# Performance work log

Measured on AMD Instinct MI355X. Metric: run time of the kernel, lower is better.

Reference implementation:

```python
import jax, jax.numpy as jnp
import numpy as np
from jax import lax

B, H, T, K = 32, 384, 1024, 3
MAX_LEN = 4096  # fixed ragged-output capacity (pad/mask for jit)
EPS = 1e-5


def conv1d_same(x, W, b):
    # x: [B,H,T], W: [H_out,H_in,K] -> [B,H,T] with SAME padding
    y = lax.conv_general_dilated(x, W, (1,), 'SAME',
                                 dimension_numbers=('NCH', 'OIH', 'NCH'))
    return y + b[None, :, None]


def layernorm_ch(x, g, b):
    # LayerNorm over the channel (hidden) dim of [B,H,T]
    m = jnp.mean(x, axis=1, keepdims=True)
    v = jnp.var(x, axis=1, keepdims=True)
    return (x - m) * lax.rsqrt(v + EPS) * g[None, :, None] + b[None, :, None]


def setup_inputs() -> dict:
    key = jax.random.key(0)
    ks = jax.random.split(key, 4)
    s = 0.02  # small init so floor(exp(relu(z))) gives modest durations
    x = jax.random.normal(ks[0], (B, H, T), dtype=jnp.float32)
    W1 = jax.random.normal(ks[1], (H, H, K), dtype=jnp.float32) * s
    W2 = jax.random.normal(ks[2], (H, H, K), dtype=jnp.float32) * s
    Wl = jax.random.normal(ks[3], (H, 1), dtype=jnp.float32) * s
    z = jnp.zeros((H,), jnp.float32)
    o = jnp.ones((H,), jnp.float32)
    return {'x': x, 'W1': W1, 'b1': z, 'g1': o, 'be1': z,
            'W2': W2, 'b2': z, 'g2': o, 'be2': z,
            'Wl': Wl, 'bl': jnp.zeros((1,), jnp.float32)}


def reference(x, W1, b1, g1, be1, W2, b2, g2, be2, Wl, bl):
    h = jax.nn.relu(layernorm_ch(conv1d_same(x, W1, b1), g1, be1))
    h = jax.nn.relu(layernorm_ch(conv1d_same(h, W2, b2), g2, be2))
    # Linear(H,1) applied per timestep, then ReLU
    z = jax.nn.relu(jnp.einsum('bht,h->bt', h, Wl[:, 0]) + bl[0])  # [B,T]
    durations = jnp.floor(jnp.exp(z)).astype(jnp.int32)            # [B,T]
    # ragged repeat_interleave along time, padded to MAX_LEN:
    cum = jnp.cumsum(durations, axis=-1)                           # [B,T]
    pos = jnp.arange(MAX_LEN)
    idx = jax.vmap(lambda c: jnp.searchsorted(c, pos, side='right'))(cum)  # [B,MAX]
    valid = (pos[None, :] < cum[:, -1:]).astype(x.dtype)           # [B,MAX]
    idx_c = jnp.minimum(idx, T - 1)
    aligned = jnp.take_along_axis(x, idx_c[:, None, :], axis=-1) * valid[:, None, :]
    return durations, aligned
```

## Files before the change

kernel.cpp:

```cpp
#include <hip/hip_runtime.h>
#include <hip/hip_bf16.h>


#define BB 32
#define HHD 384
#define TTOT 1024
#define MAXL 4096

typedef _Float16 half8 __attribute__((ext_vector_type(8)));
typedef float floatx4 __attribute__((ext_vector_type(4)));

__global__ void prep_w_kernel(const float* __restrict__ W1,
                              const float* __restrict__ W2,
                              _Float16* __restrict__ q1h, _Float16* __restrict__ q1l,
                              _Float16* __restrict__ q2h, _Float16* __restrict__ q2l) {
    const int e = blockIdx.x * 256 + threadIdx.x;
    const float* W = blockIdx.y ? W2 : W1;
    _Float16* oh = blockIdx.y ? q2h : q1h;
    _Float16* ol = blockIdx.y ? q2l : q1l;
    const int d  = e & 31;
    const int m  = (e >> 5) % 384;
    const int ck = e / (32 * 384);
    const int c  = ck / 3, k = ck - 3 * c;
    const float w = W[(size_t)m * 1152 + (size_t)(32 * c + d) * 3 + k];
    const _Float16 hi = (_Float16)w;
    oh[e] = hi;
    ol[e] = (_Float16)((w - (float)hi) * 2048.0f);
}

__global__ void prep_x_kernel(const float* __restrict__ X,
                              _Float16* __restrict__ o1,
                              _Float16* __restrict__ o2) {
    __shared__ float Ls[64][65];
    const int h0 = blockIdx.x * 64;
    const int t0 = blockIdx.y * 64;
    const int b  = blockIdx.z;
    const int tid = threadIdx.x;
    const int tl = tid & 63, hq = tid >> 6;
    const float* Xb = X + (size_t)b * HHD * TTOT;
#pragma unroll
    for (int i = 0; i < 16; ++i) {
        const int h = i * 4 + hq;
        Ls[tl][h] = Xb[(size_t)(h0 + h) * TTOT + t0 + tl];
    }
    __syncthreads();
#pragma unroll
    for (int i = 0; i < 16; ++i) {
        const int t = i * 4 + hq;
        const float v = Ls[t][tl];
        const _Float16 a = (_Float16)v;
        const size_t o = ((size_t)b * TTOT + t0 + t) * HHD + h0 + tl;
        o1[o] = a;
        o2[o] = (_Float16)((v - (float)a) * 2048.0f);
    }
}

__launch_bounds__(256, 2)
__global__ void conv_mfma_kernel(const _Float16* __restrict__ Bh,
                                 const _Float16* __restrict__ Bl,
                                 const _Float16* __restrict__ Ah,
                                 const _Float16* __restrict__ Al,
                                 const float* __restrict__ bias,
                                 float* __restrict__ Out) {
    __shared__ __align__(16) _Float16 sm[33440];
    const int tid  = threadIdx.x;
    const int lane = tid & 63, wid = tid >> 6;
    const int wm = wid >> 1, wn = wid & 1;
    const int l15 = lane & 15, g4 = lane >> 4;
    const int h0 = blockIdx.x * 96;
    const int t0 = blockIdx.y * 128;
    const int b  = blockIdx.z;

    floatx4 ahh[3][4], axx[3][4];
#pragma unroll
    for (int mt = 0; mt < 3; ++mt)
#pragma unroll
        for (int nt = 0; nt < 4; ++nt) {
            ahh[mt][nt] = (floatx4){0.f, 0.f, 0.f, 0.f};
            axx[mt][nt] = (floatx4){0.f, 0.f, 0.f, 0.f};
        }

    const size_t xbase = (size_t)b * TTOT * HHD;

    for (int ch = 0; ch < 12; ++ch) {
        __syncthreads();
#pragma unroll
        for (int it = 0; it < 9; ++it) {
            const int e  = tid + it * 256;
            const int s  = e / 1152;
            const int r1 = e - s * 1152;
            const int k  = r1 / 384;
            const int q  = r1 - k * 384;
            const int m  = q >> 2, c8 = (q & 3) << 3;
            const _Float16* src = (s ? Al : Ah) +
                ((size_t)((ch * 3 + k) * 384 + h0 + m) << 5) + c8;
            const uint4 v = *(const uint4*)src;
            *(uint4*)&sm[((s * 3 + k) * 96 + m) * 40 + c8] = v;
        }
#pragma unroll
        for (int it = 0; it < 5; ++it) {
            const int e = tid + it * 256;
            if (e < 1040) {
                const int s  = e / 520;
                const int r1 = e - s * 520;
                const int j  = r1 >> 2, q = r1 & 3;
                const int gt = t0 - 1 + j;
                uint4 v = make_uint4(0u, 0u, 0u, 0u);
                if (gt >= 0 && gt < TTOT) {
                    const _Float16* src = (s ? Bl : Bh) + xbase +
                        (size_t)gt * HHD + ch * 32 + (q << 3);
                    v = *(const uint4*)src;
                }
                *(uint4*)&sm[23040 + (s * 130 + j) * 40 + (q << 3)] = v;
            }
        }
        __syncthreads();

#pragma unroll
        for (int k = 0; k < 3; ++k) {
            half8 ah[3], al[3], bh[4], bl[4];
#pragma unroll
            for (int mt = 0; mt < 3; ++mt) {
                const int m = wm * 48 + mt * 16 + l15;
                ah[mt] = *(const half8*)&sm[((0 + k) * 96 + m) * 40 + g4 * 8];
                al[mt] = *(const half8*)&sm[((3 + k) * 96 + m) * 40 + g4 * 8];
            }
#pragma unroll
            for (int nt = 0; nt < 4; ++nt) {
                const int j = wn * 64 + nt * 16 + l15 + k;
                bh[nt] = *(const half8*)&sm[23040 + (0   + j) * 40 + g4 * 8];
                bl[nt] = *(const half8*)&sm[23040 + (130 + j) * 40 + g4 * 8];
            }
#pragma unroll
            for (int mt = 0; mt < 3; ++mt)
#pragma unroll
                for (int nt = 0; nt < 4; ++nt) {
                    ahh[mt][nt] = __builtin_amdgcn_mfma_f32_16x16x32_f16(
                        ah[mt], bh[nt], ahh[mt][nt], 0, 0, 0);
                    axx[mt][nt] = __builtin_amdgcn_mfma_f32_16x16x32_f16(
                        ah[mt], bl[nt], axx[mt][nt], 0, 0, 0);
                    axx[mt][nt] = __builtin_amdgcn_mfma_f32_16x16x32_f16(
                        al[mt], bh[nt], axx[mt][nt], 0, 0, 0);
                }
        }
    }

    __syncthreads();
    float* Lt = (float*)sm;
#pragma unroll
    for (int mt = 0; mt < 3; ++mt)
#pragma unroll
        for (int nt = 0; nt < 4; ++nt) {
            const int row = wn * 64 + nt * 16 + l15;
            const int col = wm * 48 + mt * 16 + g4 * 4;
            float4 v;
            v.x = ahh[mt][nt][0] + axx[mt][nt][0] * (1.0f / 2048.0f);
            v.y = ahh[mt][nt][1] + axx[mt][nt][1] * (1.0f / 2048.0f);
            v.z = ahh[mt][nt][2] + axx[mt][nt][2] * (1.0f / 2048.0f);
            v.w = ahh[mt][nt][3] + axx[mt][nt][3] * (1.0f / 2048.0f);
            *(float4*)&Lt[row * 100 + col] = v;
        }
    __syncthreads();
    const size_t obase = ((size_t)b * TTOT + t0) * HHD + h0;
#pragma unroll
    for (int i = 0; i < 12; ++i) {
        const int e = tid + i * 256;
        const int row = e / 24, c4 = (e - row * 24) * 4;
        float4 v = *(const float4*)&Lt[row * 100 + c4];
        const float4 bv = *(const float4*)&bias[h0 + c4];
        v.x += bv.x; v.y += bv.y; v.z += bv.z; v.w += bv.w;
        *(float4*)&Out[obase + (size_t)row * HHD + c4] = v;
    }
}

__global__ void ln_split_kernel(const float* __restrict__ hraw,
                                const float* __restrict__ g,
                                const float* __restrict__ be,
                                _Float16* __restrict__ o1,
                                _Float16* __restrict__ o2) {
    const int row = blockIdx.x * 4 + (threadIdx.x >> 6);
    const int ln  = threadIdx.x & 63;
    const float* src = hraw + (size_t)row * HHD;
    float v[6], s = 0.f, ss = 0.f;
#pragma unroll
    for (int j = 0; j < 6; ++j) { v[j] = src[ln + 64 * j]; s += v[j]; ss += v[j] * v[j]; }
#pragma unroll
    for (int m = 32; m >= 1; m >>= 1) { s += __shfl_xor(s, m, 64); ss += __shfl_xor(ss, m, 64); }
    const float mean = s * (1.f / HHD);
    const float var  = ss * (1.f / HHD) - mean * mean;
    const float inv  = rsqrtf(var + 1e-5f);
#pragma unroll
    for (int j = 0; j < 6; ++j) {
        const int h = ln + 64 * j;
        float y = (v[j] - mean) * inv * g[h] + be[h];
        y = fmaxf(y, 0.f);
        const _Float16 a = (_Float16)y;
        const size_t o = (size_t)row * HHD + h;
        o1[o] = a;
        o2[o] = (_Float16)((y - (float)a) * 2048.0f);
    }
}

__global__ void ln_proj_kernel(const float* __restrict__ hraw,
                               const float* __restrict__ g,
                               const float* __restrict__ be,
                               const float* __restrict__ Wl,
                               const float* __restrict__ blp,
                               float* __restrict__ zb) {
    const int row = blockIdx.x * 4 + (threadIdx.x >> 6);
    const int ln  = threadIdx.x & 63;
    const float* src = hraw + (size_t)row * HHD;
    float v[6], s = 0.f, ss = 0.f;
#pragma unroll
    for (int j = 0; j < 6; ++j) { v[j] = src[ln + 64 * j]; s += v[j]; ss += v[j] * v[j]; }
#pragma unroll
    for (int m = 32; m >= 1; m >>= 1) { s += __shfl_xor(s, m, 64); ss += __shfl_xor(ss, m, 64); }
    const float mean = s * (1.f / HHD);
    const float inv  = rsqrtf(ss * (1.f / HHD) - mean * mean + 1e-5f);
    float zs = 0.f;
#pragma unroll
    for (int j = 0; j < 6; ++j) {
        const int h = ln + 64 * j;
        float y = (v[j] - mean) * inv * g[h] + be[h];
        zs += fmaxf(y, 0.f) * Wl[h];
    }
#pragma unroll
    for (int m = 32; m >= 1; m >>= 1) zs += __shfl_xor(zs, m, 64);
    if (ln == 0) zb[row] = fmaxf(zs + blp[0], 0.f);
}

__global__ void dur_scan_kernel(const float* __restrict__ z,
                                float* __restrict__ durOut,
                                int* __restrict__ cum) {
    __shared__ int sb[TTOT];
    const int b = blockIdx.x;
    const int t = threadIdx.x;
    const int d = (int)floorf(expf(z[b * TTOT + t]));
    durOut[b * TTOT + t] = (float)d;
    sb[t] = d;
    __syncthreads();
    for (int off = 1; off < TTOT; off <<= 1) {
        const int v = (t >= off) ? sb[t - off] : 0;
        __syncthreads();
        sb[t] += v;
        __syncthreads();
    }
    cum[b * TTOT + t] = sb[t];
}

__global__ void gather_kernel(const float* __restrict__ X,
                              const int* __restrict__ cum,
                              float* __restrict__ aligned) {
    __shared__ int cs[TTOT];
    const int b   = blockIdx.y;
    const int tid = threadIdx.x;
    for (int e = tid; e < TTOT; e += 256) cs[e] = cum[b * TTOT + e];
    __syncthreads();
    const int pos   = blockIdx.x * 256 + tid;
    const int total = cs[TTOT - 1];
    int lo = 0, hi = TTOT;
    while (lo < hi) {
        const int mid = (lo + hi) >> 1;
        if (cs[mid] <= pos) lo = mid + 1; else hi = mid;
    }
    const float vmul = (pos < total) ? 1.f : 0.f;
    const int idx = min(lo, TTOT - 1);
    const float* Xb = X + (size_t)b * HHD * TTOT;
    float* Ab = aligned + (size_t)b * HHD * MAXL;
#pragma unroll 4
    for (int h = 0; h < HHD; ++h)
        Ab[(size_t)h * MAXL + pos] = Xb[(size_t)h * TTOT + idx] * vmul;
}

extern "C" void kernel_launch(void* const* d_in, const int* in_sizes, int n_in,
                              void* d_out, int out_size, void* d_ws, size_t ws_size,
                              hipStream_t stream) {
    const float* x   = (const float*)d_in[0];
    const float* W1  = (const float*)d_in[1];
    const float* b1  = (const float*)d_in[2];
    const float* g1  = (const float*)d_in[3];
    const float* be1 = (const float*)d_in[4];
    const float* W2  = (const float*)d_in[5];
    const float* b2  = (const float*)d_in[6];
    const float* g2  = (const float*)d_in[7];
    const float* be2 = (const float*)d_in[8];
    const float* Wl  = (const float*)d_in[9];
    const float* bl  = (const float*)d_in[10];

    float* out     = (float*)d_out;
    float* durOut  = out;
    float* aligned = out + (size_t)BB * TTOT;
    float* h_raw   = aligned;

    char* ws = (char*)d_ws;
    const size_t wqB = (size_t)442368 * sizeof(_Float16);
    const size_t xtB = (size_t)BB * TTOT * HHD * sizeof(_Float16);
    _Float16* Wq1h = (_Float16*)(ws);
    _Float16* Wq1l = (_Float16*)(ws + wqB);
    _Float16* Wq2h = (_Float16*)(ws + 2 * wqB);
    _Float16* Wq2l = (_Float16*)(ws + 3 * wqB);
    _Float16* Xt1  = (_Float16*)(ws + 4 * wqB);
    _Float16* Xt2  = (_Float16*)(ws + 4 * wqB + xtB);
    float*    zb   = (float*)   (ws + 4 * wqB + 2 * xtB);
    int*      cum  = (int*)     (ws + 4 * wqB + 2 * xtB + (size_t)BB * TTOT * 4);

    prep_w_kernel<<<dim3(1728, 2), 256, 0, stream>>>(W1, W2, Wq1h, Wq1l, Wq2h, Wq2l);
    prep_x_kernel<<<dim3(6, 16, 32), 256, 0, stream>>>(x, Xt1, Xt2);
    conv_mfma_kernel<<<dim3(4, 8, 32), 256, 0, stream>>>(Xt1, Xt2, Wq1h, Wq1l, b1, h_raw);
    ln_split_kernel<<<8192, 256, 0, stream>>>(h_raw, g1, be1, Xt1, Xt2);
    conv_mfma_kernel<<<dim3(4, 8, 32), 256, 0, stream>>>(Xt1, Xt2, Wq2h, Wq2l, b2, h_raw);
    ln_proj_kernel<<<8192, 256, 0, stream>>>(h_raw, g2, be2, Wl, bl, zb);
    dur_scan_kernel<<<BB, TTOT, 0, stream>>>(zb, durOut, cum);
    gather_kernel<<<dim3(MAXL / 256, BB), 256, 0, stream>>>(x, cum, aligned);
}
```

Baseline: 515.8 us.

## Prefetch next chunk's weight and input tiles into registers during MFMA compute

The conv GEMM kernel's global-to-LDS staging becomes register-staged software pipelining. The next channel chunk's weight and input tiles are loaded into registers while the current chunk's MFMAs run, and the address arithmetic is hoisted out of the loop. This hides global load latency behind compute at the cost of about 56 extra VGPRs per thread, which may lower occupancy.

```diff
diff --git a/kernel.cpp b/kernel.cpp
--- a/kernel.cpp
+++ b/kernel.cpp
@@ -82,39 +82,68 @@
 
     const size_t xbase = (size_t)b * TTOT * HHD;
 
+    int wdst[9];
+    const _Float16* wsrc0[9];
+#pragma unroll
+    for (int it = 0; it < 9; ++it) {
+        const int e  = tid + it * 256;
+        const int s  = e / 1152;
+        const int r1 = e - s * 1152;
+        const int k  = r1 / 384;
+        const int q  = r1 - k * 384;
+        const int m  = q >> 2, c8 = (q & 3) << 3;
+        wsrc0[it] = (s ? Al : Ah) + ((size_t)(k * 384 + h0 + m) << 5) + c8;
+        wdst[it]  = ((s * 3 + k) * 96 + m) * 40 + c8;
+    }
+    int xdst[5], xgt[5];
+    const _Float16* xsrc0[5];
+    bool xact[5];
+#pragma unroll
+    for (int it = 0; it < 5; ++it) {
+        const int e = tid + it * 256;
+        xact[it] = (e < 1040);
+        const int s  = e / 520;
+        const int r1 = e - s * 520;
+        const int j  = r1 >> 2, q = r1 & 3;
+        const int gt = t0 - 1 + j;
+        xgt[it]  = gt;
+        xsrc0[it] = (s ? Bl : Bh) + xbase + (size_t)max(gt, 0) * HHD + (q << 3);
+        xdst[it]  = 23040 + (s * 130 + j) * 40 + (q << 3);
+    }
+
+    uint4 wreg[9], xreg[5];
+#pragma unroll
+    for (int it = 0; it < 9; ++it) wreg[it] = *(const uint4*)(wsrc0[it]);
+#pragma unroll
+    for (int it = 0; it < 5; ++it) {
+        uint4 v = make_uint4(0u, 0u, 0u, 0u);
+        if (xact[it] && xgt[it] >= 0 && xgt[it] < TTOT)
+            v = *(const uint4*)(xsrc0[it]);
+        xreg[it] = v;
+    }
+
     for (int ch = 0; ch < 12; ++ch) {
         __syncthreads();
 #pragma unroll
-        for (int it = 0; it < 9; ++it) {
-            const int e  = tid + it * 256;
-            const int s  = e / 1152;
-            const int r1 = e - s * 1152;
-            const int k  = r1 / 384;
-            const int q  = r1 - k * 384;
-            const int m  = q >> 2, c8 = (q & 3) << 3;
-            const _Float16* src = (s ? Al : Ah) +
-                ((size_t)((ch * 3 + k) * 384 + h0 + m) << 5) + c8;
-            const uint4 v = *(const uint4*)src;
-            *(uint4*)&sm[((s * 3 + k) * 96 + m) * 40 + c8] = v;
-        }
-#pragma unroll
-        for (int it = 0; it < 5; ++it) {
-            const int e = tid + it * 256;
-            if (e < 1040) {
-                const int s  = e / 520;
-                const int r1 = e - s * 520;
-                const int j  = r1 >> 2, q = r1 & 3;
-                const int gt = t0 - 1 + j;
+        for (int it = 0; it < 9; ++it) *(uint4*)&sm[wdst[it]] = wreg[it];
+#pragma unroll
+        for (int it = 0; it < 5; ++it)
+            if (xact[it]) *(uint4*)&sm[xdst[it]] = xreg[it];
+        __syncthreads();
+
+        if (ch < 11) {
+            const size_t woff = (size_t)(ch + 1) * 3 * 384 * 32;
+            const int    xoff = (ch + 1) * 32;
+#pragma unroll
+            for (int it = 0; it < 9; ++it) wreg[it] = *(const uint4*)(wsrc0[it] + woff);
+#pragma unroll
+            for (int it = 0; it < 5; ++it) {
                 uint4 v = make_uint4(0u, 0u, 0u, 0u);
-                if (gt >= 0 && gt < TTOT) {
-                    const _Float16* src = (s ? Bl : Bh) + xbase +
-                        (size_t)gt * HHD + ch * 32 + (q << 3);
-                    v = *(const uint4*)src;
-                }
-                *(uint4*)&sm[23040 + (s * 130 + j) * 40 + (q << 3)] = v;
+                if (xact[it] && xgt[it] >= 0 && xgt[it] < TTOT)
+                    v = *(const uint4*)(xsrc0[it] + xoff);
+                xreg[it] = v;
             }
         }
-        __syncthreads();
 
 #pragma unroll
         for (int k = 0; k < 3; ++k) {
```

Measured after the change: 639.8 us. 24.1% more time.

## Use direct global-to-LDS loads for conv tiles and mask halo in registers

Applied to the files above, without the earlier changes.

Replaces the register-staged global→LDS copies of weight and input tiles with global_load_lds direct transfers, precomputing source pointers outside the channel loop. The LDS layout drops the 40-element padded row stride for an unpadded 32 stride, because direct loads write contiguous per-wave chunks. Out-of-range time halo rows are now loaded from clamped addresses and zeroed in registers at the MFMA operand stage. This cuts VGPR traffic and LDS footprint, but the unpadded stride may cause LDS bank conflicts on the half8 reads.

```diff
diff --git a/kernel.cpp b/kernel.cpp
--- a/kernel.cpp
+++ b/kernel.cpp
@@ -62,7 +62,7 @@
                                  const _Float16* __restrict__ Al,
                                  const float* __restrict__ bias,
                                  float* __restrict__ Out) {
-    __shared__ __align__(16) _Float16 sm[33440];
+    __shared__ __align__(16) _Float16 sm[26752];
     const int tid  = threadIdx.x;
     const int lane = tid & 63, wid = tid >> 6;
     const int wm = wid >> 1, wn = wid & 1;
@@ -70,6 +70,10 @@
     const int h0 = blockIdx.x * 96;
     const int t0 = blockIdx.y * 128;
     const int b  = blockIdx.z;
+    const int wbid = tid & 192;
+
+    const bool haloL = (blockIdx.y == 0) && (wn == 0) && (l15 == 0);
+    const bool haloH = (blockIdx.y == 7) && (wn == 1) && (l15 == 15);
 
     floatx4 ahh[3][4], axx[3][4];
 #pragma unroll
@@ -82,37 +86,51 @@
 
     const size_t xbase = (size_t)b * TTOT * HHD;
 
+    const _Float16* wsrc[9];
+#pragma unroll
+    for (int it = 0; it < 9; ++it) {
+        const int e  = tid + it * 256;
+        const int s  = e / 1152;
+        const int r1 = e - s * 1152;
+        const int k  = r1 / 384;
+        const int q  = r1 - k * 384;
+        const int m  = q >> 2, c8 = (q & 3) << 3;
+        wsrc[it] = (s ? Al : Ah) + ((size_t)(k * 384 + h0 + m) << 5) + c8;
+    }
+    const _Float16* xsrc[5];
+#pragma unroll
+    for (int it = 0; it < 5; ++it) {
+        const int e  = tid + it * 256;
+        const int s  = e / 520;
+        const int r1 = e - s * 520;
+        const int j  = r1 >> 2, q = r1 & 3;
+        const int gt  = t0 - 1 + j;
+        const int gtc = min(max(gt, 0), TTOT - 1);
+        xsrc[it] = (s ? Bl : Bh) + xbase + (size_t)gtc * HHD + (q << 3);
+    }
+
+    const half8 hz = {0, 0, 0, 0, 0, 0, 0, 0};
+
     for (int ch = 0; ch < 12; ++ch) {
         __syncthreads();
+        const size_t woff = (size_t)ch * (3 * 384 * 32);
+        const int    xoff = ch * 32;
 #pragma unroll
         for (int it = 0; it < 9; ++it) {
-            const int e  = tid + it * 256;
-            const int s  = e / 1152;
-            const int r1 = e - s * 1152;
-            const int k  = r1 / 384;
-            const int q  = r1 - k * 384;
-            const int m  = q >> 2, c8 = (q & 3) << 3;
-            const _Float16* src = (s ? Al : Ah) +
-                ((size_t)((ch * 3 + k) * 384 + h0 + m) << 5) + c8;
-            const uint4 v = *(const uint4*)src;
-            *(uint4*)&sm[((s * 3 + k) * 96 + m) * 40 + c8] = v;
-        }
-#pragma unroll
-        for (int it = 0; it < 5; ++it) {
-            const int e = tid + it * 256;
-            if (e < 1040) {
-                const int s  = e / 520;
-                const int r1 = e - s * 520;
-                const int j  = r1 >> 2, q = r1 & 3;
-                const int gt = t0 - 1 + j;
-                uint4 v = make_uint4(0u, 0u, 0u, 0u);
-                if (gt >= 0 && gt < TTOT) {
-                    const _Float16* src = (s ? Bl : Bh) + xbase +
-                        (size_t)gt * HHD + ch * 32 + (q << 3);
-                    v = *(const uint4*)src;
-                }
-                *(uint4*)&sm[23040 + (s * 130 + j) * 40 + (q << 3)] = v;
-            }
+            __builtin_amdgcn_global_load_lds(
+                (const unsigned int*)(wsrc[it] + woff),
+                (unsigned int*)&sm[(size_t)(it * 256 + wbid) * 8], 16, 0, 0);
+        }
+#pragma unroll
+        for (int it = 0; it < 4; ++it) {
+            __builtin_amdgcn_global_load_lds(
+                (const unsigned int*)(xsrc[it] + xoff),
+                (unsigned int*)&sm[18432 + (size_t)(it * 256 + wbid) * 8], 16, 0, 0);
+        }
+        if (tid < 16) {
+            __builtin_amdgcn_global_load_lds(
+                (const unsigned int*)(xsrc[4] + xoff),
+                (unsigned int*)&sm[18432 + (size_t)(4 * 256) * 8], 16, 0, 0);
         }
         __syncthreads();
 
@@ -122,15 +140,17 @@
 #pragma unroll
             for (int mt = 0; mt < 3; ++mt) {
                 const int m = wm * 48 + mt * 16 + l15;
-                ah[mt] = *(const half8*)&sm[((0 + k) * 96 + m) * 40 + g4 * 8];
-                al[mt] = *(const half8*)&sm[((3 + k) * 96 + m) * 40 + g4 * 8];
+                ah[mt] = *(const half8*)&sm[((0 + k) * 96 + m) * 32 + g4 * 8];
+                al[mt] = *(const half8*)&sm[((3 + k) * 96 + m) * 32 + g4 * 8];
             }
 #pragma unroll
             for (int nt = 0; nt < 4; ++nt) {
                 const int j = wn * 64 + nt * 16 + l15 + k;
-                bh[nt] = *(const half8*)&sm[23040 + (0   + j) * 40 + g4 * 8];
-                bl[nt] = *(const half8*)&sm[23040 + (130 + j) * 40 + g4 * 8];
+                bh[nt] = *(const half8*)&sm[18432 + (0   + j) * 32 + g4 * 8];
+                bl[nt] = *(const half8*)&sm[18432 + (130 + j) * 32 + g4 * 8];
             }
+            if (k == 0 && haloL) { bh[0] = hz; bl[0] = hz; }
+            if (k == 2 && haloH) { bh[3] = hz; bl[3] = hz; }
 #pragma unroll
             for (int mt = 0; mt < 3; ++mt)
 #pragma unroll
```

After: 484.2 us. 1.07x faster.

## Fuse conv with channel LayerNorm by giving each block all channels

Applied to the files above, without the earlier changes.

The conv kernel now computes all 384 output channels for a 32-timestep tile, so LayerNorm statistics can be reduced inside the block. The first LayerNorm, ReLU and hi/lo fp16 split are folded into the first conv's epilogue, and the second LayerNorm plus the linear projection into the second's. This removes the fp32 intermediate round-trips through global memory and two separate LN launches. Weight and activation tiles are now staged with direct global-to-LDS loads, and the weight tile is reloaded per tap with extra barriers. The trade-offs are a smaller time tile with more weight traffic per block and only 1024 blocks.

```diff
diff --git a/kernel.cpp b/kernel.cpp
--- a/kernel.cpp
+++ b/kernel.cpp
@@ -55,86 +55,103 @@
     }
 }
 
+template <int MODE>
 __launch_bounds__(256, 2)
-__global__ void conv_mfma_kernel(const _Float16* __restrict__ Bh,
-                                 const _Float16* __restrict__ Bl,
-                                 const _Float16* __restrict__ Ah,
-                                 const _Float16* __restrict__ Al,
-                                 const float* __restrict__ bias,
-                                 float* __restrict__ Out) {
-    __shared__ __align__(16) _Float16 sm[33440];
+__global__ void conv_ln_fused(const _Float16* __restrict__ Bh,
+                              const _Float16* __restrict__ Bl,
+                              const _Float16* __restrict__ Ah,
+                              const _Float16* __restrict__ Al,
+                              const float* __restrict__ bias,
+                              const float* __restrict__ gain,
+                              const float* __restrict__ beta,
+                              const float* __restrict__ Wl,
+                              const float* __restrict__ blp,
+                              _Float16* __restrict__ O1,
+                              _Float16* __restrict__ O2,
+                              float* __restrict__ zb) {
+    __shared__ __align__(16) _Float16 sm[26752];
     const int tid  = threadIdx.x;
-    const int lane = tid & 63, wid = tid >> 6;
-    const int wm = wid >> 1, wn = wid & 1;
+    const int lane = tid & 63, w = tid >> 6;
     const int l15 = lane & 15, g4 = lane >> 4;
-    const int h0 = blockIdx.x * 96;
-    const int t0 = blockIdx.y * 128;
-    const int b  = blockIdx.z;
-
-    floatx4 ahh[3][4], axx[3][4];
-#pragma unroll
-    for (int mt = 0; mt < 3; ++mt)
-#pragma unroll
-        for (int nt = 0; nt < 4; ++nt) {
+    const int tt = blockIdx.x;
+    const int t0 = tt * 32;
+    const int b  = blockIdx.y;
+
+    floatx4 ahh[6][2], axx[6][2];
+#pragma unroll
+    for (int mt = 0; mt < 6; ++mt)
+#pragma unroll
+        for (int nt = 0; nt < 2; ++nt) {
             ahh[mt][nt] = (floatx4){0.f, 0.f, 0.f, 0.f};
             axx[mt][nt] = (floatx4){0.f, 0.f, 0.f, 0.f};
         }
 
     const size_t xbase = (size_t)b * TTOT * HHD;
-
-    for (int ch = 0; ch < 12; ++ch) {
-        __syncthreads();
-#pragma unroll
-        for (int it = 0; it < 9; ++it) {
-            const int e  = tid + it * 256;
-            const int s  = e / 1152;
-            const int r1 = e - s * 1152;
-            const int k  = r1 / 384;
-            const int q  = r1 - k * 384;
-            const int m  = q >> 2, c8 = (q & 3) << 3;
-            const _Float16* src = (s ? Al : Ah) +
-                ((size_t)((ch * 3 + k) * 384 + h0 + m) << 5) + c8;
-            const uint4 v = *(const uint4*)src;
-            *(uint4*)&sm[((s * 3 + k) * 96 + m) * 40 + c8] = v;
-        }
-#pragma unroll
-        for (int it = 0; it < 5; ++it) {
-            const int e = tid + it * 256;
-            if (e < 1040) {
-                const int s  = e / 520;
-                const int r1 = e - s * 520;
-                const int j  = r1 >> 2, q = r1 & 3;
-                const int gt = t0 - 1 + j;
-                uint4 v = make_uint4(0u, 0u, 0u, 0u);
-                if (gt >= 0 && gt < TTOT) {
-                    const _Float16* src = (s ? Bl : Bh) + xbase +
-                        (size_t)gt * HHD + ch * 32 + (q << 3);
-                    v = *(const uint4*)src;
+    const half8 hz = {0, 0, 0, 0, 0, 0, 0, 0};
+
+    for (int c = 0; c < 12; ++c) {
+        __syncthreads();
+        {
+            int e = tid;
+            if (e < 272) {
+                const int s = (e >= 136);
+                const int r = e - s * 136;
+                const int gtc = min(max(t0 - 1 + (r >> 2), 0), TTOT - 1);
+                const _Float16* src = (s ? Bl : Bh) + xbase +
+                    (size_t)gtc * HHD + c * 32 + ((r & 3) << 3);
+                __builtin_amdgcn_global_load_lds((const unsigned int*)src,
+                    (unsigned int*)&sm[24576 + e * 8], 16, 0, 0);
+            }
+            e = 256 + tid;
+            if (tid < 16) {
+                const int r = e - 136;
+                const int gtc = min(max(t0 - 1 + (r >> 2), 0), TTOT - 1);
+                const _Float16* src = Bl + xbase +
+                    (size_t)gtc * HHD + c * 32 + ((r & 3) << 3);
+                __builtin_amdgcn_global_load_lds((const unsigned int*)src,
+                    (unsigned int*)&sm[24576 + e * 8], 16, 0, 0);
+            }
+        }
+        for (int k = 0; k < 3; ++k) {
+            if (k > 0) __syncthreads();
+            {
+                const size_t wo = (size_t)(c * 3 + k) * 12288;
+#pragma unroll
+                for (int it = 0; it < 6; ++it) {
+                    const int r = tid + it * 256;
+                    __builtin_amdgcn_global_load_lds(
+                        (const unsigned int*)(Ah + wo + r * 8),
+                        (unsigned int*)&sm[r * 8], 16, 0, 0);
                 }
-                *(uint4*)&sm[23040 + (s * 130 + j) * 40 + (q << 3)] = v;
-            }
-        }
-        __syncthreads();
-
-#pragma unroll
-        for (int k = 0; k < 3; ++k) {
-            half8 ah[3], al[3], bh[4], bl[4];
-#pragma unroll
-            for (int mt = 0; mt < 3; ++mt) {
-                const int m = wm * 48 + mt * 16 + l15;
-                ah[mt] = *(const half8*)&sm[((0 + k) * 96 + m) * 40 + g4 * 8];
-                al[mt] = *(const half8*)&sm[((3 + k) * 96 + m) * 40 + g4 * 8];
-            }
-#pragma unroll
-            for (int nt = 0; nt < 4; ++nt) {
-                const int j = wn * 64 + nt * 16 + l15 + k;
-                bh[nt] = *(const half8*)&sm[23040 + (0   + j) * 40 + g4 * 8];
-                bl[nt] = *(const half8*)&sm[23040 + (130 + j) * 40 + g4 * 8];
-            }
-#pragma unroll
-            for (int mt = 0; mt < 3; ++mt)
-#pragma unroll
-                for (int nt = 0; nt < 4; ++nt) {
+#pragma unroll
+                for (int it = 0; it < 6; ++it) {
+                    const int r = tid + it * 256;
+                    __builtin_amdgcn_global_load_lds(
+                        (const unsigned int*)(Al + wo + r * 8),
+                        (unsigned int*)&sm[12288 + r * 8], 16, 0, 0);
+                }
+            }
+            __syncthreads();
+
+            half8 ah[6], al[6], bh[2], bl[2];
+#pragma unroll
+            for (int mt = 0; mt < 6; ++mt) {
+                const int m = w * 96 + mt * 16 + l15;
+                ah[mt] = *(const half8*)&sm[m * 32 + g4 * 8];
+                al[mt] = *(const half8*)&sm[12288 + m * 32 + g4 * 8];
+            }
+#pragma unroll
+            for (int nt = 0; nt < 2; ++nt) {
+                const int j = nt * 16 + l15 + k;
+                bh[nt] = *(const half8*)&sm[24576 + j * 32 + g4 * 8];
+                bl[nt] = *(const half8*)&sm[24576 + 1088 + j * 32 + g4 * 8];
+            }
+            if (tt == 0 && k == 0 && l15 == 0)  { bh[0] = hz; bl[0] = hz; }
+            if (tt == 31 && k == 2 && l15 == 15) { bh[1] = hz; bl[1] = hz; }
+#pragma unroll
+            for (int mt = 0; mt < 6; ++mt)
+#pragma unroll
+                for (int nt = 0; nt < 2; ++nt) {
                     ahh[mt][nt] = __builtin_amdgcn_mfma_f32_16x16x32_f16(
                         ah[mt], bh[nt], ahh[mt][nt], 0, 0, 0);
                     axx[mt][nt] = __builtin_amdgcn_mfma_f32_16x16x32_f16(
@@ -146,87 +163,125 @@
     }
 
     __syncthreads();
-    float* Lt = (float*)sm;
-#pragma unroll
-    for (int mt = 0; mt < 3; ++mt)
-#pragma unroll
-        for (int nt = 0; nt < 4; ++nt) {
-            const int row = wn * 64 + nt * 16 + l15;
-            const int col = wm * 48 + mt * 16 + g4 * 4;
-            float4 v;
-            v.x = ahh[mt][nt][0] + axx[mt][nt][0] * (1.0f / 2048.0f);
-            v.y = ahh[mt][nt][1] + axx[mt][nt][1] * (1.0f / 2048.0f);
-            v.z = ahh[mt][nt][2] + axx[mt][nt][2] * (1.0f / 2048.0f);
-            v.w = ahh[mt][nt][3] + axx[mt][nt][3] * (1.0f / 2048.0f);
-            *(float4*)&Lt[row * 100 + col] = v;
-        }
-    __syncthreads();
-    const size_t obase = ((size_t)b * TTOT + t0) * HHD + h0;
-#pragma unroll
-    for (int i = 0; i < 12; ++i) {
-        const int e = tid + i * 256;
-        const int row = e / 24, c4 = (e - row * 24) * 4;
-        float4 v = *(const float4*)&Lt[row * 100 + c4];
-        const float4 bv = *(const float4*)&bias[h0 + c4];
-        v.x += bv.x; v.y += bv.y; v.z += bv.z; v.w += bv.w;
-        *(float4*)&Out[obase + (size_t)row * HHD + c4] = v;
-    }
-}
-
-__global__ void ln_split_kernel(const float* __restrict__ hraw,
-                                const float* __restrict__ g,
-                                const float* __restrict__ be,
-                                _Float16* __restrict__ o1,
-                                _Float16* __restrict__ o2) {
-    const int row = blockIdx.x * 4 + (threadIdx.x >> 6);
-    const int ln  = threadIdx.x & 63;
-    const float* src = hraw + (size_t)row * HHD;
-    float v[6], s = 0.f, ss = 0.f;
-#pragma unroll
-    for (int j = 0; j < 6; ++j) { v[j] = src[ln + 64 * j]; s += v[j]; ss += v[j] * v[j]; }
-#pragma unroll
-    for (int m = 32; m >= 1; m >>= 1) { s += __shfl_xor(s, m, 64); ss += __shfl_xor(ss, m, 64); }
-    const float mean = s * (1.f / HHD);
-    const float var  = ss * (1.f / HHD) - mean * mean;
-    const float inv  = rsqrtf(var + 1e-5f);
-#pragma unroll
-    for (int j = 0; j < 6; ++j) {
-        const int h = ln + 64 * j;
-        float y = (v[j] - mean) * inv * g[h] + be[h];
-        y = fmaxf(y, 0.f);
-        const _Float16 a = (_Float16)y;
-        const size_t o = (size_t)row * HHD + h;
-        o1[o] = a;
-        o2[o] = (_Float16)((y - (float)a) * 2048.0f);
-    }
-}
-
-__global__ void ln_proj_kernel(const float* __restrict__ hraw,
-                               const float* __restrict__ g,
-                               const float* __restrict__ be,
-                               const float* __restrict__ Wl,
-                               const float* __restrict__ blp,
-                               float* __restrict__ zb) {
-    const int row = blockIdx.x * 4 + (threadIdx.x >> 6);
-    const int ln  = threadIdx.x & 63;
-    const float* src = hraw + (size_t)row * HHD;
-    float v[6], s = 0.f, ss = 0.f;
-#pragma unroll
-    for (int j = 0; j < 6; ++j) { v[j] = src[ln + 64 * j]; s += v[j]; ss += v[j] * v[j]; }
-#pragma unroll
-    for (int m = 32; m >= 1; m >>= 1) { s += __shfl_xor(s, m, 64); ss += __shfl_xor(ss, m, 64); }
-    const float mean = s * (1.f / HHD);
-    const float inv  = rsqrtf(ss * (1.f / HHD) - mean * mean + 1e-5f);
-    float zs = 0.f;
-#pragma unroll
-    for (int j = 0; j < 6; ++j) {
-        const int h = ln + 64 * j;
-        float y = (v[j] - mean) * inv * g[h] + be[h];
-        zs += fmaxf(y, 0.f) * Wl[h];
-    }
-#pragma unroll
-    for (int m = 32; m >= 1; m >>= 1) zs += __shfl_xor(zs, m, 64);
-    if (ln == 0) zb[row] = fmaxf(zs + blp[0], 0.f);
+    float* st = (float*)sm;
+
+#pragma unroll
+    for (int mt = 0; mt < 6; ++mt) {
+        const float4 bv = *(const float4*)&bias[w * 96 + mt * 16 + g4 * 4];
+#pragma unroll
+        for (int nt = 0; nt < 2; ++nt)
+#pragma unroll
+            for (int r = 0; r < 4; ++r)
+                ahh[mt][nt][r] += axx[mt][nt][r] * (1.0f / 2048.0f) +
+                                  ((const float*)&bv)[r];
+    }
+    float s0 = 0.f, ss0 = 0.f, s1 = 0.f, ss1 = 0.f;
+#pragma unroll
+    for (int mt = 0; mt < 6; ++mt)
+#pragma unroll
+        for (int r = 0; r < 4; ++r) {
+            const float v0 = ahh[mt][0][r], v1 = ahh[mt][1][r];
+            s0 += v0; ss0 += v0 * v0;
+            s1 += v1; ss1 += v1 * v1;
+        }
+    s0 += __shfl_xor(s0, 16, 64); ss0 += __shfl_xor(ss0, 16, 64);
+    s1 += __shfl_xor(s1, 16, 64); ss1 += __shfl_xor(ss1, 16, 64);
+    s0 += __shfl_xor(s0, 32, 64); ss0 += __shfl_xor(ss0, 32, 64);
+    s1 += __shfl_xor(s1, 32, 64); ss1 += __shfl_xor(ss1, 32, 64);
+    if (g4 == 0) {
+        st[(l15 * 4 + w) * 2]            = s0;
+        st[(l15 * 4 + w) * 2 + 1]        = ss0;
+        st[((16 + l15) * 4 + w) * 2]     = s1;
+        st[((16 + l15) * 4 + w) * 2 + 1] = ss1;
+    }
+    __syncthreads();
+    float mean[2], inv[2];
+#pragma unroll
+    for (int nt = 0; nt < 2; ++nt) {
+        const int t = nt * 16 + l15;
+        float s = 0.f, ss = 0.f;
+#pragma unroll
+        for (int wv = 0; wv < 4; ++wv) {
+            s  += st[(t * 4 + wv) * 2];
+            ss += st[(t * 4 + wv) * 2 + 1];
+        }
+        const float m = s * (1.0f / HHD);
+        mean[nt] = m;
+        inv[nt]  = rsqrtf(ss * (1.0f / HHD) - m * m + 1e-5f);
+    }
+
+    if constexpr (MODE == 0) {
+        float* Lt = (float*)sm + 512;
+#pragma unroll
+        for (int mt = 0; mt < 6; ++mt) {
+            const int hb = w * 96 + mt * 16 + g4 * 4;
+            const float4 ga = *(const float4*)&gain[hb];
+            const float4 be = *(const float4*)&beta[hb];
+#pragma unroll
+            for (int nt = 0; nt < 2; ++nt) {
+                const int t = nt * 16 + l15;
+                float4 y;
+#pragma unroll
+                for (int r = 0; r < 4; ++r) {
+                    float v = (ahh[mt][nt][r] - mean[nt]) * inv[nt] *
+                              ((const float*)&ga)[r] + ((const float*)&be)[r];
+                    ((float*)&y)[r] = fmaxf(v, 0.f);
+                }
+                *(float4*)&Lt[t * 392 + hb] = y;
+            }
+        }
+        __syncthreads();
+#pragma unroll
+        for (int i = 0; i < 6; ++i) {
+            const int cc = tid + i * 256;
+            const int row = cc / 48, hc = cc - row * 48;
+            const float4 aq = *(const float4*)&Lt[row * 392 + hc * 8];
+            const float4 bq = *(const float4*)&Lt[row * 392 + hc * 8 + 4];
+            half8 vh, vl;
+#pragma unroll
+            for (int j = 0; j < 4; ++j) {
+                const float f0 = ((const float*)&aq)[j];
+                const float f1 = ((const float*)&bq)[j];
+                const _Float16 a0 = (_Float16)f0, a1 = (_Float16)f1;
+                vh[j]     = a0; vl[j]     = (_Float16)((f0 - (float)a0) * 2048.0f);
+                vh[j + 4] = a1; vl[j + 4] = (_Float16)((f1 - (float)a1) * 2048.0f);
+            }
+            const size_t o = ((size_t)b * TTOT + t0 + row) * HHD + hc * 8;
+            *(half8*)&O1[o] = vh;
+            *(half8*)&O2[o] = vl;
+        }
+    } else {
+        float zs0 = 0.f, zs1 = 0.f;
+#pragma unroll
+        for (int mt = 0; mt < 6; ++mt) {
+            const int hb = w * 96 + mt * 16 + g4 * 4;
+            const float4 ga = *(const float4*)&gain[hb];
+            const float4 be = *(const float4*)&beta[hb];
+            const float4 wl = *(const float4*)&Wl[hb];
+#pragma unroll
+            for (int r = 0; r < 4; ++r) {
+                const float y0 = fmaxf((ahh[mt][0][r] - mean[0]) * inv[0] *
+                    ((const float*)&ga)[r] + ((const float*)&be)[r], 0.f);
+                const float y1 = fmaxf((ahh[mt][1][r] - mean[1]) * inv[1] *
+                    ((const float*)&ga)[r] + ((const float*)&be)[r], 0.f);
+                zs0 += y0 * ((const float*)&wl)[r];
+                zs1 += y1 * ((const float*)&wl)[r];
+            }
+        }
+        zs0 += __shfl_xor(zs0, 16, 64); zs1 += __shfl_xor(zs1, 16, 64);
+        zs0 += __shfl_xor(zs0, 32, 64); zs1 += __shfl_xor(zs1, 32, 64);
+        float* zp = (float*)sm + 256;
+        if (g4 == 0) {
+            zp[l15 * 4 + w]        = zs0;
+            zp[(16 + l15) * 4 + w] = zs1;
+        }
+        __syncthreads();
+        if (tid < 32) {
+            const float zsum = zp[tid * 4] + zp[tid * 4 + 1] +
+                               zp[tid * 4 + 2] + zp[tid * 4 + 3];
+            zb[b * TTOT + t0 + tid] = fmaxf(zsum + blp[0], 0.f);
+        }
+    }
 }
 
 __global__ void dur_scan_kernel(const float* __restrict__ z,
@@ -290,7 +345,6 @@
     float* out     = (float*)d_out;
     float* durOut  = out;
     float* aligned = out + (size_t)BB * TTOT;
-    float* h_raw   = aligned;
 
     char* ws = (char*)d_ws;
     const size_t wqB = (size_t)442368 * sizeof(_Float16);
@@ -301,15 +355,17 @@
     _Float16* Wq2l = (_Float16*)(ws + 3 * wqB);
     _Float16* Xt1  = (_Float16*)(ws + 4 * wqB);
     _Float16* Xt2  = (_Float16*)(ws + 4 * wqB + xtB);
-    float*    zb   = (float*)   (ws + 4 * wqB + 2 * xtB);
-    int*      cum  = (int*)     (ws + 4 * wqB + 2 * xtB + (size_t)BB * TTOT * 4);
+    _Float16* H1t1 = (_Float16*)(ws + 4 * wqB + 2 * xtB);
+    _Float16* H1t2 = (_Float16*)(ws + 4 * wqB + 3 * xtB);
+    float*    zb   = (float*)   (ws + 4 * wqB + 4 * xtB);
+    int*      cum  = (int*)     (ws + 4 * wqB + 4 * xtB + (size_t)BB * TTOT * 4);
 
     prep_w_kernel<<<dim3(1728, 2), 256, 0, stream>>>(W1, W2, Wq1h, Wq1l, Wq2h, Wq2l);
     prep_x_kernel<<<dim3(6, 16, 32), 256, 0, stream>>>(x, Xt1, Xt2);
-    conv_mfma_kernel<<<dim3(4, 8, 32), 256, 0, stream>>>(Xt1, Xt2, Wq1h, Wq1l, b1, h_raw);
-    ln_split_kernel<<<8192, 256, 0, stream>>>(h_raw, g1, be1, Xt1, Xt2);
-    conv_mfma_kernel<<<dim3(4, 8, 32), 256, 0, stream>>>(Xt1, Xt2, Wq2h, Wq2l, b2, h_raw);
-    ln_proj_kernel<<<8192, 256, 0, stream>>>(h_raw, g2, be2, Wl, bl, zb);
+    conv_ln_fused<0><<<dim3(32, BB), 256, 0, stream>>>(
+        Xt1, Xt2, Wq1h, Wq1l, b1, g1, be1, nullptr, nullptr, H1t1, H1t2, nullptr);
+    conv_ln_fused<1><<<dim3(32, BB), 256, 0, stream>>>(
+        H1t1, H1t2, Wq2h, Wq2l, b2, g2, be2, Wl, bl, nullptr, nullptr, zb);
     dur_scan_kernel<<<BB, TTOT, 0, stream>>>(zb, durOut, cum);
     gather_kernel<<<dim3(MAXL / 256, BB), 256, 0, stream>>>(x, cum, aligned);
 }
```

Result: faster. 492.3 us (-4.5%).
